# Optimization experiments

Measured on AMD Instinct MI355X. Metric: run time of the kernel, lower is better.

The kernel has to match this reference:

```python
import jax, jax.numpy as jnp
import numpy as np

G = 16          # grid_size
B = 2           # num graphs
SPACING = 1.5   # anchor_spacing
KA = 8          # atom_k_neighbors
KG = 24         # k_neighbors (grid->atom)
CUTOFF = 8.0
T = 16          # n_atom_types
H = 240         # hidden irreps dim (64x0e+32x1o+16x2e)
A = 9           # SH attr dim, lmax=2
C = 32          # code_dim
L = 2           # num_layers
BIG = 1e9

# real spherical harmonics, 'integral' normalization, e3nn component order
C0 = 0.28209479177387814   # 1/(2 sqrt(pi))
C1 = 0.4886025119029199    # sqrt(3/(4 pi))
C2A = 1.0925484305920792   # sqrt(15/(4 pi))
C2B = 0.31539156525252005  # sqrt(5/(16 pi))
C2C = 0.5462742152960396   # sqrt(15/(16 pi))

def _sph(rel, dist):
    u = rel / jnp.maximum(dist, 1e-9)[:, None]
    x, y, z = u[:, 0], u[:, 1], u[:, 2]
    return jnp.stack([
        jnp.full_like(x, C0),
        C1 * y, C1 * z, C1 * x,
        C2A * x * y, C2A * y * z, C2B * (3.0 * z * z - 1.0),
        C2A * z * x, C2C * (x * x - y * y),
    ], axis=-1)


def setup_inputs():
    key = jax.random.key(0)
    ks = jax.random.split(key, 12)
    Na = 1024
    half = G * SPACING / 2.0
    pos = jax.random.uniform(ks[0], (Na, 3), minval=-half, maxval=half, dtype=jnp.float32)
    atom_types = jax.random.randint(ks[1], (Na,), 0, T, dtype=jnp.int32)
    atom_batch = jnp.repeat(jnp.arange(B, dtype=jnp.int32), Na // B)

    def lin(k, shape):
        fan_in = shape[-2]
        return jax.random.normal(k, shape, dtype=jnp.float32) / jnp.sqrt(float(fan_in))

    Din = 2 * H + A
    return dict(
        pos=pos, atom_types=atom_types, atom_batch=atom_batch,
        We=lin(ks[2], (T + A, H)), be=jnp.zeros((H,), jnp.float32),
        Wm1=lin(ks[3], (L, Din, H)), bm1=jnp.zeros((L, H), jnp.float32),
        Wm2=lin(ks[4], (L, H, H)), bm2=jnp.zeros((L, H), jnp.float32),
        Wu1=lin(ks[5], (L, Din, H)), bu1=jnp.zeros((L, H), jnp.float32),
        Wu2=lin(ks[6], (L, H, H)), bu2=jnp.zeros((L, H), jnp.float32),
        Wo1=lin(ks[7], (H, H)), bo1=jnp.zeros((H,), jnp.float32),
        Wo2=lin(ks[8], (H, C)), bo2=jnp.zeros((C,), jnp.float32),
    )


def _forward(pos, atom_types, atom_batch, We, be, Wm1, bm1, Wm2, bm2,
             Wu1, bu1, Wu2, bu2, Wo1, bo1, Wo2, bo2):
    Na = pos.shape[0]
    ng = G ** 3
    Ng = B * ng
    N = Na + Ng

    # anchor grid, centered, spacing SPACING
    ax = (jnp.arange(G, dtype=pos.dtype) - (G - 1) / 2.0) * SPACING
    grid = jnp.stack(jnp.meshgrid(ax, ax, ax, indexing='ij'), -1).reshape(-1, 3)  # [ng,3]
    grid_flat = jnp.tile(grid, (B, 1))                                            # [Ng,3]
    grid_batch = jnp.repeat(jnp.arange(B, dtype=atom_batch.dtype), ng)
    node_pos = jnp.concatenate([pos, grid_flat], 0)                               # [N,3]

    # atom-atom knn_graph (no self loops, per-graph)
    d2 = jnp.sum((pos[:, None] - pos[None]) ** 2, -1)                             # [Na,Na]
    d2 = jnp.where(atom_batch[:, None] == atom_batch[None], d2, BIG)
    d2 = jnp.where(jnp.eye(Na, dtype=bool), BIG, d2)
    _, nbr = jax.lax.top_k(-d2, KA)                                               # [Na,KA]

    # grid->atom knn (per-graph), edge src=atom, dst=grid node
    d2g = jnp.sum((grid_flat[:, None] - pos[None]) ** 2, -1)                      # [Ng,Na]
    d2g = jnp.where(grid_batch[:, None] == atom_batch[None], d2g, BIG)
    _, nbg = jax.lax.top_k(-d2g, KG)                                              # [Ng,KG]

    src = jnp.concatenate([nbr.reshape(-1), nbg.reshape(-1)])
    dst = jnp.concatenate([jnp.repeat(jnp.arange(Na), KA),
                           Na + jnp.repeat(jnp.arange(Ng), KG)])

    rel = node_pos[src] - node_pos[dst]
    dist = jnp.linalg.norm(rel, axis=-1)
    mask = (dist <= CUTOFF).astype(pos.dtype)        # cutoff as mask (jit-friendly)
    ea = _sph(rel, dist) * mask[:, None]             # [E,A]

    # node attrs: scatter-mean of edge SH over destination nodes
    na_sum = jax.ops.segment_sum(ea, dst, num_segments=N)
    cnt = jax.ops.segment_sum(mask, dst, num_segments=N)
    node_attr = na_sum / jnp.maximum(cnt, 1.0)[:, None]
    node_attr = node_attr.at[:, 0].set(1.0)

    # node features: one-hot atoms, zeros for anchors
    feat = jnp.concatenate([jax.nn.one_hot(atom_types, T, dtype=pos.dtype),
                            jnp.zeros((Ng, T), pos.dtype)], 0)
    h = jax.nn.silu(jnp.concatenate([feat, node_attr], -1) @ We + be)

    # SEGNN-style message passing (attr-conditioned MLPs, masked-sum aggregation)
    for l in range(L):
        mi = jnp.concatenate([h[src], h[dst], ea], -1)                            # [E,2H+A]
        m = jax.nn.silu(jax.nn.silu(mi @ Wm1[l] + bm1[l]) @ Wm2[l] + bm2[l])
        m = m * mask[:, None]
        agg = jax.ops.segment_sum(m, dst, num_segments=N)                         # [N,H]
        ui = jnp.concatenate([h, agg, node_attr], -1)                             # [N,2H+A]
        h = h + jax.nn.silu(jax.nn.silu(ui @ Wu1[l] + bu1[l]) @ Wu2[l] + bu2[l])

    out = jax.nn.silu(h @ Wo1 + bo1) @ Wo2 + bo2                                  # [N,C]
    return out[Na:].reshape(B, ng, C)


def reference(pos, atom_types, atom_batch, We, be, Wm1, bm1, Wm2, bm2,
              Wu1, bu1, Wu2, bu2, Wo1, bo1, Wo2, bo2):
    return _forward(pos, atom_types, atom_batch, We, be, Wm1, bm1, Wm2, bm2,
                    Wu1, bu1, Wu2, bu2, Wo1, bo1, Wo2, bo2)
```

## Files before the change

### kernel.cpp

```cpp
#include <hip/hip_runtime.h>
#include <math.h>

#define NA   1024
#define NGRID 4096
#define NB   2
#define NG   (NB*NGRID)
#define NN   (NA+NG)
#define KAK  8
#define KGK  24
#define EAE  (NA*KAK)
#define EGE  (NG*KGK)
#define ET   (EAE+EGE)
#define HD   240
#define TT   16
#define DIN  489
#define CD   32
#define CUTF 8.0f

typedef __attribute__((ext_vector_type(8))) short short8;
typedef __attribute__((ext_vector_type(4))) short short4v;
typedef __attribute__((ext_vector_type(4))) float f32x4;
typedef __attribute__((ext_vector_type(4))) int i32x4;

__device__ __forceinline__ float silu_f(float x) {
    return x / (1.0f + __expf(-x));
}
__device__ __forceinline__ short f2bf(float x) {
    unsigned u = __float_as_uint(x);
    unsigned r = (u + 0x7FFFu + ((u >> 16) & 1u)) >> 16;
    return (short)r;
}
__device__ __forceinline__ float bf2f(short s) {
    return __uint_as_float(((unsigned)(unsigned short)s) << 16);
}
__device__ __forceinline__ unsigned cvt_pk_bf16(float lo, float hi) {
    unsigned r;
    asm("v_cvt_pk_bf16_f32 %0, %1, %2" : "=v"(r) : "v"(lo), "v"(hi));
    return r;
}

template <int K>
__device__ __forceinline__ void wave_topk(unsigned long long key[8], int lane,
                                          int* __restrict__ outp) {
    unsigned long long lmin = key[0];
#pragma unroll
    for (int s = 1; s < 8; ++s) lmin = key[s] < lmin ? key[s] : lmin;
    int myout = -1;
    for (int t = 0; t < K; ++t) {
        unsigned long long m = lmin;
#pragma unroll
        for (int d = 1; d < 64; d <<= 1) {
            unsigned long long o = __shfl_xor(m, d);
            m = o < m ? o : m;
        }
        if (lane == t) myout = (int)(m & 1023u);
        if (m == lmin) {
#pragma unroll
            for (int s = 0; s < 8; ++s) if (key[s] == m) key[s] = ~0ull;
            lmin = key[0];
#pragma unroll
            for (int s = 1; s < 8; ++s) lmin = key[s] < lmin ? key[s] : lmin;
        }
    }
    if (lane < K) outp[lane] = myout;
}

__global__ __launch_bounds__(256) void knn_atoms_kernel(const float* __restrict__ pos,
                                                        int* __restrict__ nbr) {
    __shared__ float sx[512], sy[512], sz[512];
    int tid = threadIdx.x;
    int q0 = blockIdx.x * 4;
    int pbase = (q0 >= 512) ? 512 : 0;
    for (int j = tid; j < 512; j += 256) {
        sx[j] = pos[(pbase + j)*3 + 0];
        sy[j] = pos[(pbase + j)*3 + 1];
        sz[j] = pos[(pbase + j)*3 + 2];
    }
    __syncthreads();
    int lane = tid & 63;
    int i = q0 + (tid >> 6);
    float px = sx[i - pbase], py = sy[i - pbase], pz = sz[i - pbase];
    unsigned long long key[8];
#pragma unroll
    for (int s = 0; s < 8; ++s) {
        int c = s * 64 + lane;
        int j = pbase + c;
        float dx = px - sx[c], dy = py - sy[c], dz = pz - sz[c];
        float d2 = __fadd_rn(__fadd_rn(__fmul_rn(dx,dx), __fmul_rn(dy,dy)), __fmul_rn(dz,dz));
        key[s] = ((unsigned long long)__float_as_uint(d2) << 10) | (unsigned)j;
        if (j == i) key[s] = ~0ull;
    }
    wave_topk<KAK>(key, lane, &nbr[i*KAK]);
}

__global__ __launch_bounds__(256) void knn_grid_kernel(const float* __restrict__ pos,
                                                       int* __restrict__ nbg) {
    __shared__ float sx[512], sy[512], sz[512];
    int tid = threadIdx.x;
    int q0 = blockIdx.x * 4;
    int pbase = (q0 >= NGRID) ? 512 : 0;
    for (int j = tid; j < 512; j += 256) {
        sx[j] = pos[(pbase + j)*3 + 0];
        sy[j] = pos[(pbase + j)*3 + 1];
        sz[j] = pos[(pbase + j)*3 + 2];
    }
    __syncthreads();
    int lane = tid & 63;
    int g = q0 + (tid >> 6);
    int gi = g & (NGRID - 1);
    int ix = gi >> 8, iy = (gi >> 4) & 15, iz = gi & 15;
    float px = ((float)ix - 7.5f) * 1.5f;
    float py = ((float)iy - 7.5f) * 1.5f;
    float pz = ((float)iz - 7.5f) * 1.5f;
    unsigned long long key[8];
#pragma unroll
    for (int s = 0; s < 8; ++s) {
        int c = s * 64 + lane;
        int j = pbase + c;
        float dx = px - sx[c], dy = py - sy[c], dz = pz - sz[c];
        float d2 = __fadd_rn(__fadd_rn(__fmul_rn(dx,dx), __fmul_rn(dy,dy)), __fmul_rn(dz,dz));
        key[s] = ((unsigned long long)__float_as_uint(d2) << 10) | (unsigned)j;
    }
    wave_topk<KGK>(key, lane, &nbg[g*KGK]);
}

__global__ void edge_kernel(const float* __restrict__ pos, const int* __restrict__ nbr,
                            const int* __restrict__ nbg, float* __restrict__ ea,
                            float* __restrict__ emask) {
    int e = blockIdx.x * blockDim.x + threadIdx.x;
    if (e >= ET) return;
    int src; float dpx, dpy, dpz;
    if (e < EAE) {
        int d = e >> 3;
        src = nbr[e];
        dpx = pos[d*3]; dpy = pos[d*3+1]; dpz = pos[d*3+2];
    } else {
        int eg = e - EAE;
        src = nbg[eg];
        int gg = eg / KGK;
        int gi = gg % NGRID;
        int ix = gi >> 8, iy = (gi >> 4) & 15, iz = gi & 15;
        dpx = ((float)ix - 7.5f) * 1.5f;
        dpy = ((float)iy - 7.5f) * 1.5f;
        dpz = ((float)iz - 7.5f) * 1.5f;
    }
    float rx = pos[src*3] - dpx, ry = pos[src*3+1] - dpy, rz = pos[src*3+2] - dpz;
    float dist = sqrtf(rx*rx + ry*ry + rz*rz);
    float mask = (dist <= CUTF) ? 1.0f : 0.0f;
    float inv = 1.0f / fmaxf(dist, 1e-9f);
    float x = rx * inv, y = ry * inv, z = rz * inv;
    float s0 = 0.28209479177387814f;
    float s1 = 0.4886025119029199f * y;
    float s2 = 0.4886025119029199f * z;
    float s3 = 0.4886025119029199f * x;
    float s4 = 1.0925484305920792f * x * y;
    float s5 = 1.0925484305920792f * y * z;
    float s6 = 0.31539156525252005f * (3.0f * z * z - 1.0f);
    float s7 = 1.0925484305920792f * z * x;
    float s8 = 0.5462742152960396f * (x * x - y * y);
    float* o = &ea[(size_t)e * 12];
    float4 o0 = {s0*mask, s1*mask, s2*mask, s3*mask};
    float4 o1 = {s4*mask, s5*mask, s6*mask, s7*mask};
    float4 o2 = {s8*mask, 0.f, 0.f, 0.f};
    *(float4*)(o)     = o0;
    *(float4*)(o + 4) = o1;
    *(float4*)(o + 8) = o2;
    emask[e] = mask;
}

__global__ void node_attr_kernel(const float* __restrict__ ea, const float* __restrict__ emask,
                                 float* __restrict__ attr) {
    int n = blockIdx.x * blockDim.x + threadIdx.x;
    if (n >= NN) return;
    int K, e0;
    if (n < NA) { K = KAK; e0 = n * KAK; }
    else        { K = KGK; e0 = EAE + (n - NA) * KGK; }
    float s[9];
#pragma unroll
    for (int a = 0; a < 9; ++a) s[a] = 0.f;
    float cnt = 0.f;
    for (int k = 0; k < K; ++k) {
        cnt += emask[e0 + k];
        const float* p = &ea[(size_t)(e0 + k) * 12];
#pragma unroll
        for (int a = 0; a < 9; ++a) s[a] += p[a];
    }
    float invc = 1.0f / fmaxf(cnt, 1.0f);
    attr[n*9+0] = 1.0f;
#pragma unroll
    for (int a = 1; a < 9; ++a) attr[n*9+a] = s[a] * invc;
}

__global__ void encoder_kernel(const int* __restrict__ types, const float* __restrict__ attr,
                               const float* __restrict__ We, const float* __restrict__ be,
                               float* __restrict__ h) {
    int idx = blockIdx.x * blockDim.x + threadIdx.x;
    int n = idx / HD, j = idx % HD;
    float acc = be[j];
    if (n < NA) acc += We[types[n] * HD + j];
#pragma unroll
    for (int a = 0; a < 9; ++a) acc += attr[n*9+a] * We[(TT + a) * HD + j];
    h[idx] = silu_f(acc);
}

__global__ void convert_w_kernel(const float* __restrict__ src, short* __restrict__ dst,
                                 int K, int Kpad) {
    int idx = blockIdx.x * blockDim.x + threadIdx.x;
    int per = 256 * Kpad;
    int l = idx / per;
    int rem = idx % per;
    int col = rem / Kpad, k = rem % Kpad;
    short v = 0;
    if (k < K && col < 240) v = f2bf(src[(size_t)l * K * 240 + (size_t)k * 240 + col]);
    dst[idx] = v;
}

__global__ void convert_wm1hl_kernel(const float* __restrict__ Wm1, short* __restrict__ hi,
                                     short* __restrict__ lo, int rowoff) {
    int idx = blockIdx.x * blockDim.x + threadIdx.x;
    int l = idx >> 16;
    int rem = idx & 65535;
    int col = rem >> 8, k = rem & 255;
    float v = 0.f;
    if (k < 240 && col < 240) v = Wm1[(size_t)l * DIN * HD + (size_t)(rowoff + k) * HD + col];
    short h16 = f2bf(v);
    hi[idx] = h16;
    lo[idx] = f2bf(v - bf2f(h16));
}

__global__ __launch_bounds__(256) void node_z_mfma_kernel(
        const float* __restrict__ h,
        const short* __restrict__ wzd_hi, const short* __restrict__ wzd_lo,
        const short* __restrict__ wzs_hi, const short* __restrict__ wzs_lo,
        const float* __restrict__ bm1,
        float* __restrict__ Zs, float* __restrict__ Zd) {
    __shared__ __align__(16) short Ahi[32 * 256];
    __shared__ __align__(16) short Alo[32 * 256];
    int tid = threadIdx.x;
    int n0 = blockIdx.x * 32;

#pragma unroll
    for (int it = 0; it < 4; ++it) {
        int idx = it * 256 + tid;
        int row = idx >> 5, q = idx & 31;
        int j = q * 8;
        short8 ohi = {0,0,0,0,0,0,0,0}, olo = {0,0,0,0,0,0,0,0};
        if (j < 240) {
            const float4 a0 = *(const float4*)(h + (size_t)(n0 + row) * HD + j);
            const float4 a1 = *(const float4*)(h + (size_t)(n0 + row) * HD + j + 4);
            float v[8] = {a0.x, a0.y, a0.z, a0.w, a1.x, a1.y, a1.z, a1.w};
#pragma unroll
            for (int a = 0; a < 8; ++a) {
                short hh = f2bf(v[a]);
                ohi[a] = hh;
                olo[a] = f2bf(v[a] - bf2f(hh));
            }
        }
        int boff = row * 512 + ((q * 16) ^ ((row & 7) << 4));
        *(short8*)((char*)Ahi + boff) = ohi;
        *(short8*)((char*)Alo + boff) = olo;
    }
    __syncthreads();

    int wid = tid >> 6, lane = tid & 63;
    int mw = wid >> 1, nw = wid & 1;
    int lg = lane >> 4, lc = lane & 15;
    int col0 = nw * 128;
    int arow = (mw * 16 + lc) * 256;

    f32x4 acc[8];
#pragma unroll
    for (int nt = 0; nt < 8; ++nt) acc[nt] = (f32x4){0.f, 0.f, 0.f, 0.f};
#pragma unroll
    for (int kc = 0; kc < 8; ++kc) {
        int aoff = arow + ((kc * 32 + lg * 8) ^ ((lc & 7) << 3));
        const short8 ahi = *(const short8*)&Ahi[aoff];
        const short8 alo = *(const short8*)&Alo[aoff];
#pragma unroll
        for (int nt = 0; nt < 8; ++nt) {
            size_t bo = (size_t)(col0 + nt*16 + lc) * 256 + kc*32 + lg*8;
            const short8 bhi = *(const short8*)(wzd_hi + bo);
            const short8 blo = *(const short8*)(wzd_lo + bo);
            acc[nt] = __builtin_amdgcn_mfma_f32_16x16x32_bf16(ahi, bhi, acc[nt], 0, 0, 0);
            acc[nt] = __builtin_amdgcn_mfma_f32_16x16x32_bf16(ahi, blo, acc[nt], 0, 0, 0);
            acc[nt] = __builtin_amdgcn_mfma_f32_16x16x32_bf16(alo, bhi, acc[nt], 0, 0, 0);
        }
    }
#pragma unroll
    for (int nt = 0; nt < 8; ++nt) {
        int ncol = col0 + nt * 16 + lc;
        if (ncol < HD) {
            float bias = bm1[ncol];
            float vals[4] = {acc[nt].x, acc[nt].y, acc[nt].z, acc[nt].w};
#pragma unroll
            for (int r = 0; r < 4; ++r)
                Zd[(size_t)(n0 + mw*16 + lg*4 + r) * HD + ncol] = vals[r] + bias;
        }
    }

    if (n0 < NA) {
#pragma unroll
        for (int nt = 0; nt < 8; ++nt) acc[nt] = (f32x4){0.f, 0.f, 0.f, 0.f};
#pragma unroll
        for (int kc = 0; kc < 8; ++kc) {
            int aoff = arow + ((kc * 32 + lg * 8) ^ ((lc & 7) << 3));
            const short8 ahi = *(const short8*)&Ahi[aoff];
            const short8 alo = *(const short8*)&Alo[aoff];
#pragma unroll
            for (int nt = 0; nt < 8; ++nt) {
                size_t bo = (size_t)(col0 + nt*16 + lc) * 256 + kc*32 + lg*8;
                const short8 bhi = *(const short8*)(wzs_hi + bo);
                const short8 blo = *(const short8*)(wzs_lo + bo);
                acc[nt] = __builtin_amdgcn_mfma_f32_16x16x32_bf16(ahi, bhi, acc[nt], 0, 0, 0);
                acc[nt] = __builtin_amdgcn_mfma_f32_16x16x32_bf16(ahi, blo, acc[nt], 0, 0, 0);
                acc[nt] = __builtin_amdgcn_mfma_f32_16x16x32_bf16(alo, bhi, acc[nt], 0, 0, 0);
            }
        }
#pragma unroll
        for (int nt = 0; nt < 8; ++nt) {
            int ncol = col0 + nt * 16 + lc;
            if (ncol < HD) {
                float vals[4] = {acc[nt].x, acc[nt].y, acc[nt].z, acc[nt].w};
#pragma unroll
                for (int r = 0; r < 4; ++r)
                    Zs[(size_t)(n0 + mw*16 + lg*4 + r) * HD + ncol] = vals[r];
            }
        }
    }
}

__global__ __launch_bounds__(256) void msg_gemm_kernel(
        const float* __restrict__ Zs, const float* __restrict__ Zd,
        const int* __restrict__ nbg, const float* __restrict__ ea,
        const float* __restrict__ emask, const float* __restrict__ Wea,
        const short* __restrict__ wm2t, const float* __restrict__ bm2,
        float* __restrict__ agg) {
    __shared__ __align__(16) short Abuf[48 * 256];
    __shared__ __align__(16) float mkbuf[48];
    int tid = threadIdx.x;
    int blk = blockIdx.x;
    int e0 = blk * 48;

    int q = tid & 31;
    int rh = tid >> 5;
    float4 w0[9], w1[9];
    int srcs[6];
    if (q < 30) {
        int j = q * 8;
#pragma unroll
        for (int a = 0; a < 9; ++a) {
            w0[a] = *(const float4*)(Wea + a * HD + j);
            w1[a] = *(const float4*)(Wea + a * HD + j + 4);
        }
#pragma unroll
        for (int r8 = 0; r8 < 6; ++r8) srcs[r8] = nbg[e0 + rh + r8 * 8];
    }
    if (tid < 48) mkbuf[tid] = emask[EAE + e0 + tid];

#pragma unroll
    for (int r8 = 0; r8 < 6; ++r8) {
        int row = rh + r8 * 8;
        i32x4 oi = (i32x4){0, 0, 0, 0};
        if (q < 30) {
            int j = q * 8;
            int eg = e0 + row;
            int srcn = srcs[r8];
            int dstn = NA + blk * 2 + ((r8 >= 3) ? 1 : 0);
            const float4 zs0 = *(const float4*)(Zs + (size_t)srcn * HD + j);
            const float4 zs1 = *(const float4*)(Zs + (size_t)srcn * HD + j + 4);
            const float4 zd0 = *(const float4*)(Zd + (size_t)dstn * HD + j);
            const float4 zd1 = *(const float4*)(Zd + (size_t)dstn * HD + j + 4);
            float s0 = zs0.x + zd0.x, s1 = zs0.y + zd0.y, s2 = zs0.z + zd0.z, s3 = zs0.w + zd0.w;
            float s4 = zs1.x + zd1.x, s5 = zs1.y + zd1.y, s6 = zs1.z + zd1.z, s7 = zs1.w + zd1.w;
            const float* ep = ea + (size_t)(EAE + eg) * 12;
            const float4 ev0 = *(const float4*)(ep);
            const float4 ev1 = *(const float4*)(ep + 4);
            const float  ev8 = ep[8];
            float ev[9] = {ev0.x, ev0.y, ev0.z, ev0.w, ev1.x, ev1.y, ev1.z, ev1.w, ev8};
#pragma unroll
            for (int a = 0; a < 9; ++a) {
                float e = ev[a];
                s0 += e * w0[a].x; s1 += e * w0[a].y; s2 += e * w0[a].z; s3 += e * w0[a].w;
                s4 += e * w1[a].x; s5 += e * w1[a].y; s6 += e * w1[a].z; s7 += e * w1[a].w;
            }
            oi[0] = (int)cvt_pk_bf16(silu_f(s0), silu_f(s1));
            oi[1] = (int)cvt_pk_bf16(silu_f(s2), silu_f(s3));
            oi[2] = (int)cvt_pk_bf16(silu_f(s4), silu_f(s5));
            oi[3] = (int)cvt_pk_bf16(silu_f(s6), silu_f(s7));
        }
        *(i32x4*)((char*)Abuf + row * 512 + ((q * 16) ^ ((row & 7) << 4))) = oi;
    }
    __syncthreads();

    int wid = tid >> 6, lane = tid & 63;
    int lg = lane >> 4, lc = lane & 15;
    int col0 = wid * 64;

    f32x4 acc[3][4];
#pragma unroll
    for (int mt = 0; mt < 3; ++mt)
#pragma unroll
        for (int nt = 0; nt < 4; ++nt) acc[mt][nt] = (f32x4){0.f, 0.f, 0.f, 0.f};

#pragma unroll
    for (int kc = 0; kc < 8; ++kc) {
        short8 af[3];
#pragma unroll
        for (int mt = 0; mt < 3; ++mt)
            af[mt] = *(const short8*)&Abuf[(mt*16 + lc) * 256 +
                                           ((kc*32 + lg*8) ^ ((lc & 7) << 3))];
#pragma unroll
        for (int nt = 0; nt < 4; ++nt) {
            const short8 bf = *(const short8*)(wm2t + (size_t)(col0 + nt*16 + lc) * 256 + kc*32 + lg*8);
#pragma unroll
            for (int mt = 0; mt < 3; ++mt)
                acc[mt][nt] = __builtin_amdgcn_mfma_f32_16x16x32_bf16(af[mt], bf, acc[mt][nt], 0, 0, 0);
        }
    }

#pragma unroll
    for (int nt = 0; nt < 4; ++nt) {
        int ncol = col0 + nt * 16 + lc;
        float bias = (ncol < HD) ? bm2[ncol] : 0.f;
        float p[3];
#pragma unroll
        for (int mt = 0; mt < 3; ++mt) {
            const float4 mkv = *(const float4*)&mkbuf[mt*16 + lg*4];
            float t0 = silu_f(acc[mt][nt].x + bias) * mkv.x;
            float t1 = silu_f(acc[mt][nt].y + bias) * mkv.y;
            float t2 = silu_f(acc[mt][nt].z + bias) * mkv.z;
            float t3 = silu_f(acc[mt][nt].w + bias) * mkv.w;
            p[mt] = (t0 + t1) + (t2 + t3);
        }
        float v0 = p[0] + ((lg < 2) ? p[1] : 0.f);
        float v1 = ((lg >= 2) ? p[1] : 0.f) + p[2];
        v0 += __shfl_xor(v0, 16); v0 += __shfl_xor(v0, 32);
        v1 += __shfl_xor(v1, 16); v1 += __shfl_xor(v1, 32);
        if (ncol < HD) {
            int node = NA + blk * 2;
            if (lane < 16)      agg[(size_t)(node + 0) * HD + ncol] = v0;
            else if (lane < 32) agg[(size_t)(node + 1) * HD + ncol] = v1;
        }
    }
}

template <int KE, int NPB>
__global__ __launch_bounds__(192) void msg_mfma_kernel(
        const float* __restrict__ Zs, const float* __restrict__ Zd,
        const int* __restrict__ nbrList, const float* __restrict__ ea,
        const float* __restrict__ emask, const float* __restrict__ Wea,
        const short* __restrict__ wm2t, const float* __restrict__ bm2,
        float* __restrict__ agg, int dstBase, int edgeBase) {
    constexpr int ROWS = KE * NPB;
    constexpr int MT = ROWS / 16;
    __shared__ __align__(16) short Abuf[ROWS * 264];
    __shared__ __align__(16) float mkbuf[ROWS];

    int tid = threadIdx.x;
    int b = blockIdx.x;
    int e0 = edgeBase + b * ROWS;

    if (tid < ROWS) mkbuf[tid] = emask[e0 + tid];
    for (int idx = tid; idx < ROWS * 24; idx += 192) {
        int r = idx / 24;
        Abuf[r * 264 + 240 + (idx % 24)] = 0;
    }
    for (int idx = tid; idx < ROWS * 60; idx += 192) {
        int row = idx / 60;
        int j = (idx % 60) * 4;
        int srcn = nbrList[b * ROWS + row];
        int dstn = dstBase + b * NPB + row / KE;
        const float4 zs = *(const float4*)(Zs + (size_t)srcn * HD + j);
        const float4 zd = *(const float4*)(Zd + (size_t)dstn * HD + j);
        float s0 = zs.x + zd.x, s1 = zs.y + zd.y, s2 = zs.z + zd.z, s3 = zs.w + zd.w;
        const float* ep = ea + (size_t)(e0 + row) * 12;
#pragma unroll
        for (int a = 0; a < 9; ++a) {
            float ev = ep[a];
            const float4 w = *(const float4*)(Wea + a * HD + j);
            s0 += ev * w.x; s1 += ev * w.y; s2 += ev * w.z; s3 += ev * w.w;
        }
        short4v o;
        o.x = f2bf(silu_f(s0)); o.y = f2bf(silu_f(s1));
        o.z = f2bf(silu_f(s2)); o.w = f2bf(silu_f(s3));
        *(short4v*)&Abuf[row * 264 + j] = o;
    }
    __syncthreads();

    int w = tid / 64, lane = tid % 64;
    int lg = lane >> 4, lc = lane & 15;
    int wcol0 = w * 80;

    f32x4 acc[MT][5];
#pragma unroll
    for (int mt = 0; mt < MT; ++mt)
#pragma unroll
        for (int nt = 0; nt < 5; ++nt) acc[mt][nt] = (f32x4){0.f, 0.f, 0.f, 0.f};

#pragma unroll
    for (int kc = 0; kc < 8; ++kc) {
        short8 af[MT];
#pragma unroll
        for (int mt = 0; mt < MT; ++mt)
            af[mt] = *(const short8*)&Abuf[(mt * 16 + lc) * 264 + kc * 32 + lg * 8];
#pragma unroll
        for (int nt = 0; nt < 5; ++nt) {
            const short8 bf = *(const short8*)(wm2t + (size_t)(wcol0 + nt * 16 + lc) * 256 + kc * 32 + lg * 8);
#pragma unroll
            for (int mt = 0; mt < MT; ++mt)
                acc[mt][nt] = __builtin_amdgcn_mfma_f32_16x16x32_bf16(af[mt], bf, acc[mt][nt], 0, 0, 0);
        }
    }

#pragma unroll
    for (int nt = 0; nt < 5; ++nt) {
        int ncol = wcol0 + nt * 16 + lc;
        float bias = bm2[ncol];
        float p[MT];
#pragma unroll
        for (int mt = 0; mt < MT; ++mt) {
            const float4 mkv = *(const float4*)&mkbuf[mt * 16 + lg * 4];
            float t0 = silu_f(acc[mt][nt].x + bias) * mkv.x;
            float t1 = silu_f(acc[mt][nt].y + bias) * mkv.y;
            float t2 = silu_f(acc[mt][nt].z + bias) * mkv.z;
            float t3 = silu_f(acc[mt][nt].w + bias) * mkv.w;
            p[mt] = (t0 + t1) + (t2 + t3);
        }
#pragma unroll
        for (int mt = 0; mt < MT; ++mt) {
            float v = p[mt];
            v += __shfl_xor(v, 16);
            if (lane < 16)
                agg[(size_t)(dstBase + b * (2 * MT) + 2 * mt + 0) * HD + ncol] = v;
            else if (lane >= 32 && lane < 48)
                agg[(size_t)(dstBase + b * (2 * MT) + 2 * mt + 1) * HD + ncol] = v;
        }
    }
}

__global__ __launch_bounds__(256) void update_mfma_kernel(
        float* __restrict__ h, const float* __restrict__ agg,
        const float* __restrict__ attr,
        const short* __restrict__ wu1t, const float* __restrict__ bu1,
        const short* __restrict__ wu2t, const float* __restrict__ bu2) {
    __shared__ __align__(16) short Abuf[32 * 512];
    __shared__ __align__(16) short Ubuf[32 * 256];
    int tid = threadIdx.x;
    int n0 = blockIdx.x * 32;

#pragma unroll
    for (int it = 0; it < 8; ++it) {
        int idx = it * 256 + tid;
        int row = idx >> 6, q = idx & 63;
        int j = q * 8;
        int n = n0 + row;
        short8 o = {0,0,0,0,0,0,0,0};
        if (j < 240) {
            const float4 a0 = *(const float4*)(h + (size_t)n * HD + j);
            const float4 a1 = *(const float4*)(h + (size_t)n * HD + j + 4);
            o[0]=f2bf(a0.x); o[1]=f2bf(a0.y); o[2]=f2bf(a0.z); o[3]=f2bf(a0.w);
            o[4]=f2bf(a1.x); o[5]=f2bf(a1.y); o[6]=f2bf(a1.z); o[7]=f2bf(a1.w);
        } else if (j < 480) {
            const float4 a0 = *(const float4*)(agg + (size_t)n * HD + (j - 240));
            const float4 a1 = *(const float4*)(agg + (size_t)n * HD + (j - 240) + 4);
            o[0]=f2bf(a0.x); o[1]=f2bf(a0.y); o[2]=f2bf(a0.z); o[3]=f2bf(a0.w);
            o[4]=f2bf(a1.x); o[5]=f2bf(a1.y); o[6]=f2bf(a1.z); o[7]=f2bf(a1.w);
        } else if (j == 480) {
#pragma unroll
            for (int a = 0; a < 8; ++a) o[a] = f2bf(attr[n*9 + a]);
        } else if (j == 488) {
            o[0] = f2bf(attr[n*9 + 8]);
        }
        *(short8*)((char*)Abuf + row * 1024 + ((q * 16) ^ ((row & 7) << 4))) = o;
    }
    __syncthreads();

    int wid = tid >> 6, lane = tid & 63;
    int mw = wid >> 1, nw = wid & 1;
    int lg = lane >> 4, lc = lane & 15;
    int col0 = nw * 128;

    f32x4 acc[8];
#pragma unroll
    for (int nt = 0; nt < 8; ++nt) acc[nt] = (f32x4){0.f, 0.f, 0.f, 0.f};
#pragma unroll
    for (int kc = 0; kc < 16; ++kc) {
        const short8 af = *(const short8*)((char*)Abuf + (mw*16 + lc) * 1024 +
                                           ((kc*64 + lg*16) ^ ((lc & 7) << 4)));
#pragma unroll
        for (int nt = 0; nt < 8; ++nt) {
            const short8 bf = *(const short8*)(wu1t + (size_t)(col0 + nt*16 + lc) * 512 + kc*32 + lg*8);
            acc[nt] = __builtin_amdgcn_mfma_f32_16x16x32_bf16(af, bf, acc[nt], 0, 0, 0);
        }
    }
#pragma unroll
    for (int nt = 0; nt < 8; ++nt) {
        int ncol = col0 + nt * 16 + lc;
        float bias = (ncol < HD) ? bu1[ncol] : 0.f;
        float vals[4] = {acc[nt].x, acc[nt].y, acc[nt].z, acc[nt].w};
#pragma unroll
        for (int r = 0; r < 4; ++r) {
            int row = mw*16 + lg*4 + r;
            *(short*)((char*)Ubuf + row * 512 + ((ncol * 2) ^ ((row & 7) << 4))) =
                f2bf(silu_f(vals[r] + bias));
        }
    }
    __syncthreads();

    f32x4 acc2[8];
#pragma unroll
    for (int nt = 0; nt < 8; ++nt) acc2[nt] = (f32x4){0.f, 0.f, 0.f, 0.f};
#pragma unroll
    for (int kc = 0; kc < 8; ++kc) {
        const short8 af = *(const short8*)((char*)Ubuf + (mw*16 + lc) * 512 +
                                           ((kc*64 + lg*16) ^ ((lc & 7) << 4)));
#pragma unroll
        for (int nt = 0; nt < 8; ++nt) {
            const short8 bf = *(const short8*)(wu2t + (size_t)(col0 + nt*16 + lc) * 256 + kc*32 + lg*8);
            acc2[nt] = __builtin_amdgcn_mfma_f32_16x16x32_bf16(af, bf, acc2[nt], 0, 0, 0);
        }
    }
#pragma unroll
    for (int nt = 0; nt < 8; ++nt) {
        int ncol = col0 + nt * 16 + lc;
        if (ncol < HD) {
            float bias = bu2[ncol];
            float vals[4] = {acc2[nt].x, acc2[nt].y, acc2[nt].z, acc2[nt].w};
#pragma unroll
            for (int r = 0; r < 4; ++r) {
                int row = mw*16 + lg*4 + r;
                size_t hi = (size_t)(n0 + row) * HD + ncol;
                h[hi] += silu_f(vals[r] + bias);
            }
        }
    }
}

__global__ void output_kernel(const float* __restrict__ h,
                              const float* __restrict__ Wo1, const float* __restrict__ bo1,
                              const float* __restrict__ Wo2, const float* __restrict__ bo2,
                              float* __restrict__ out) {
    const int NBT = 4;
    __shared__ float hr[NBT][HD];
    __shared__ float o1[NBT][HD];
    int tid = threadIdx.x;
    int g0 = blockIdx.x * NBT;
    for (int idx = tid; idx < NBT * HD; idx += 256) {
        int k = idx / HD, i = idx % HD;
        hr[k][i] = h[(size_t)(NA + g0 + k) * HD + i];
    }
    __syncthreads();
    int j = tid;
    if (j < HD) {
        float acc[NBT] = {0.f, 0.f, 0.f, 0.f};
        for (int i4 = 0; i4 < 60; ++i4) {
            int i = 4 * i4;
            float w0 = Wo1[(i+0)*HD+j], w1 = Wo1[(i+1)*HD+j];
            float w2 = Wo1[(i+2)*HD+j], w3 = Wo1[(i+3)*HD+j];
#pragma unroll
            for (int k = 0; k < NBT; ++k) {
                const float4 a = *reinterpret_cast<const float4*>(&hr[k][i]);
                acc[k] += a.x*w0 + a.y*w1 + a.z*w2 + a.w*w3;
            }
        }
        float bb = bo1[j];
#pragma unroll
        for (int k = 0; k < NBT; ++k) o1[k][j] = silu_f(acc[k] + bb);
    }
    __syncthreads();
    if (tid < NBT * CD) {
        int k = tid >> 5, c = tid & 31;
        float acc = bo2[c];
        for (int i = 0; i < HD; ++i) acc += o1[k][i] * Wo2[i*CD + c];
        out[(size_t)(g0 + k) * CD + c] = acc;
    }
}

extern "C" void kernel_launch(void* const* d_in, const int* in_sizes, int n_in,
                              void* d_out, int out_size, void* d_ws, size_t ws_size,
                              hipStream_t stream) {
    (void)in_sizes; (void)n_in; (void)out_size; (void)ws_size;
    const float* pos   = (const float*)d_in[0];
    const int*   types = (const int*)d_in[1];
    const int*   batch = (const int*)d_in[2];
    (void)batch;
    const float* We    = (const float*)d_in[3];
    const float* be    = (const float*)d_in[4];
    const float* Wm1   = (const float*)d_in[5];
    const float* bm1   = (const float*)d_in[6];
    const float* Wm2   = (const float*)d_in[7];
    const float* bm2   = (const float*)d_in[8];
    const float* Wu1   = (const float*)d_in[9];
    const float* bu1   = (const float*)d_in[10];
    const float* Wu2   = (const float*)d_in[11];
    const float* bu2   = (const float*)d_in[12];
    const float* Wo1   = (const float*)d_in[13];
    const float* bo1   = (const float*)d_in[14];
    const float* Wo2   = (const float*)d_in[15];
    const float* bo2   = (const float*)d_in[16];
    float* out = (float*)d_out;

    char* ws = (char*)d_ws;
    size_t off = 0;
    auto take = [&](size_t bytes) -> char* {
        char* p = ws + off;
        off = (off + bytes + 255) & ~(size_t)255;
        return p;
    };
    int*   nbr    = (int*)take((size_t)EAE * 4);
    int*   nbg    = (int*)take((size_t)EGE * 4);
    float* ea     = (float*)take((size_t)ET * 12 * 4);
    float* emask  = (float*)take((size_t)ET * 4);
    float* attr   = (float*)take((size_t)NN * 9 * 4);
    float* h      = (float*)take((size_t)NN * HD * 4);
    float* agg    = (float*)take((size_t)NN * HD * 4);
    float* zs     = (float*)take((size_t)NA * HD * 4);
    float* zd     = (float*)take((size_t)NN * HD * 4);
    short* wm2t   = (short*)take((size_t)2 * 256 * 256 * 2);
    short* wu1t   = (short*)take((size_t)2 * 256 * 512 * 2);
    short* wu2t   = (short*)take((size_t)2 * 256 * 256 * 2);
    short* wzd_hi = (short*)take((size_t)2 * 256 * 256 * 2);
    short* wzd_lo = (short*)take((size_t)2 * 256 * 256 * 2);
    short* wzs_hi = (short*)take((size_t)2 * 256 * 256 * 2);
    short* wzs_lo = (short*)take((size_t)2 * 256 * 256 * 2);

    knn_atoms_kernel<<<NA/4, 256, 0, stream>>>(pos, nbr);
    knn_grid_kernel<<<NG/4, 256, 0, stream>>>(pos, nbg);
    edge_kernel<<<ET/256, 256, 0, stream>>>(pos, nbr, nbg, ea, emask);
    node_attr_kernel<<<NN/256, 256, 0, stream>>>(ea, emask, attr);
    encoder_kernel<<<(NN*HD)/256, 256, 0, stream>>>(types, attr, We, be, h);
    convert_w_kernel<<<(2*256*256)/256, 256, 0, stream>>>(Wm2, wm2t, 240, 256);
    convert_w_kernel<<<(2*256*512)/256, 256, 0, stream>>>(Wu1, wu1t, DIN, 512);
    convert_w_kernel<<<(2*256*256)/256, 256, 0, stream>>>(Wu2, wu2t, 240, 256);
    convert_wm1hl_kernel<<<(2*256*256)/256, 256, 0, stream>>>(Wm1, wzd_hi, wzd_lo, 240);
    convert_wm1hl_kernel<<<(2*256*256)/256, 256, 0, stream>>>(Wm1, wzs_hi, wzs_lo, 0);

    for (int l = 0; l < 2; ++l) {
        const float* wm1 = Wm1 + (size_t)l * DIN * HD;
        const float* wea = wm1 + (size_t)480 * HD;
        const short* w2t = wm2t + (size_t)l * 256 * 256;
        const float* bb2 = bm2 + l * HD;
        node_z_mfma_kernel<<<NN/32, 256, 0, stream>>>(
            h,
            wzd_hi + (size_t)l * 65536, wzd_lo + (size_t)l * 65536,
            wzs_hi + (size_t)l * 65536, wzs_lo + (size_t)l * 65536,
            bm1 + l * HD, zs, zd);
        msg_mfma_kernel<KAK, 8><<<NA*KAK/64, 192, 0, stream>>>(
            zs, zd, nbr, ea, emask, wea, w2t, bb2, agg, 0, 0);
        msg_gemm_kernel<<<EGE/48, 256, 0, stream>>>(zs, zd, nbg, ea, emask, wea, w2t, bb2, agg);
        update_mfma_kernel<<<NN/32, 256, 0, stream>>>(
            h, agg, attr,
            wu1t + (size_t)l * 256 * 512, bu1 + l * HD,
            wu2t + (size_t)l * 256 * 256, bu2 + l * HD);
    }
    output_kernel<<<NG/4, 256, 0, stream>>>(h, Wo1, bo1, Wo2, bo2, out);
}
```

Before: 661.5 us.

## Merge kNN and weight-conversion launches, pack edge attrs to 9 floats, hoist Zd loads

Combines the atom and grid kNN kernels into one launch and the five weight-conversion kernels into a single kernel, cutting launch count and per-launch overhead. Edge attributes are stored with a stride of 9 floats instead of 12, which shrinks that buffer but replaces the aligned float4 accesses with scalar ones. In the grid message kernel, the two destination Zd rows are loaded once per thread up front rather than reloaded for every row.

Result: faster. 626.0 us (-5.4%).

```diff
diff --git a/kernel.cpp b/kernel.cpp
--- a/kernel.cpp
+++ b/kernel.cpp
@@ -65,12 +65,16 @@
     if (lane < K) outp[lane] = myout;
 }
 
-__global__ __launch_bounds__(256) void knn_atoms_kernel(const float* __restrict__ pos,
-                                                        int* __restrict__ nbr) {
+__global__ __launch_bounds__(256) void knn_kernel(const float* __restrict__ pos,
+                                                  int* __restrict__ nbr,
+                                                  int* __restrict__ nbg) {
     __shared__ float sx[512], sy[512], sz[512];
     int tid = threadIdx.x;
-    int q0 = blockIdx.x * 4;
-    int pbase = (q0 >= 512) ? 512 : 0;
+    bool isAtom = blockIdx.x < (NA / 4);
+    int q0 = isAtom ? blockIdx.x * 4 : (blockIdx.x - NA / 4) * 4;
+    int pbase;
+    if (isAtom) pbase = (q0 >= 512) ? 512 : 0;
+    else        pbase = (q0 >= NGRID) ? 512 : 0;
     for (int j = tid; j < 512; j += 256) {
         sx[j] = pos[(pbase + j)*3 + 0];
         sy[j] = pos[(pbase + j)*3 + 1];
@@ -78,50 +82,39 @@
     }
     __syncthreads();
     int lane = tid & 63;
-    int i = q0 + (tid >> 6);
-    float px = sx[i - pbase], py = sy[i - pbase], pz = sz[i - pbase];
-    unsigned long long key[8];
-#pragma unroll
-    for (int s = 0; s < 8; ++s) {
-        int c = s * 64 + lane;
-        int j = pbase + c;
-        float dx = px - sx[c], dy = py - sy[c], dz = pz - sz[c];
-        float d2 = __fadd_rn(__fadd_rn(__fmul_rn(dx,dx), __fmul_rn(dy,dy)), __fmul_rn(dz,dz));
-        key[s] = ((unsigned long long)__float_as_uint(d2) << 10) | (unsigned)j;
-        if (j == i) key[s] = ~0ull;
-    }
-    wave_topk<KAK>(key, lane, &nbr[i*KAK]);
-}
-
-__global__ __launch_bounds__(256) void knn_grid_kernel(const float* __restrict__ pos,
-                                                       int* __restrict__ nbg) {
-    __shared__ float sx[512], sy[512], sz[512];
-    int tid = threadIdx.x;
-    int q0 = blockIdx.x * 4;
-    int pbase = (q0 >= NGRID) ? 512 : 0;
-    for (int j = tid; j < 512; j += 256) {
-        sx[j] = pos[(pbase + j)*3 + 0];
-        sy[j] = pos[(pbase + j)*3 + 1];
-        sz[j] = pos[(pbase + j)*3 + 2];
-    }
-    __syncthreads();
-    int lane = tid & 63;
-    int g = q0 + (tid >> 6);
-    int gi = g & (NGRID - 1);
-    int ix = gi >> 8, iy = (gi >> 4) & 15, iz = gi & 15;
-    float px = ((float)ix - 7.5f) * 1.5f;
-    float py = ((float)iy - 7.5f) * 1.5f;
-    float pz = ((float)iz - 7.5f) * 1.5f;
-    unsigned long long key[8];
-#pragma unroll
-    for (int s = 0; s < 8; ++s) {
-        int c = s * 64 + lane;
-        int j = pbase + c;
-        float dx = px - sx[c], dy = py - sy[c], dz = pz - sz[c];
-        float d2 = __fadd_rn(__fadd_rn(__fmul_rn(dx,dx), __fmul_rn(dy,dy)), __fmul_rn(dz,dz));
-        key[s] = ((unsigned long long)__float_as_uint(d2) << 10) | (unsigned)j;
-    }
-    wave_topk<KGK>(key, lane, &nbg[g*KGK]);
+    int qq = q0 + (tid >> 6);
+    if (isAtom) {
+        int i = qq;
+        float px = sx[i - pbase], py = sy[i - pbase], pz = sz[i - pbase];
+        unsigned long long key[8];
+#pragma unroll
+        for (int s = 0; s < 8; ++s) {
+            int c = s * 64 + lane;
+            int j = pbase + c;
+            float dx = px - sx[c], dy = py - sy[c], dz = pz - sz[c];
+            float d2 = __fadd_rn(__fadd_rn(__fmul_rn(dx,dx), __fmul_rn(dy,dy)), __fmul_rn(dz,dz));
+            key[s] = ((unsigned long long)__float_as_uint(d2) << 10) | (unsigned)j;
+            if (j == i) key[s] = ~0ull;
+        }
+        wave_topk<KAK>(key, lane, &nbr[i*KAK]);
+    } else {
+        int g = qq;
+        int gi = g & (NGRID - 1);
+        int ix = gi >> 8, iy = (gi >> 4) & 15, iz = gi & 15;
+        float px = ((float)ix - 7.5f) * 1.5f;
+        float py = ((float)iy - 7.5f) * 1.5f;
+        float pz = ((float)iz - 7.5f) * 1.5f;
+        unsigned long long key[8];
+#pragma unroll
+        for (int s = 0; s < 8; ++s) {
+            int c = s * 64 + lane;
+            int j = pbase + c;
+            float dx = px - sx[c], dy = py - sy[c], dz = pz - sz[c];
+            float d2 = __fadd_rn(__fadd_rn(__fmul_rn(dx,dx), __fmul_rn(dy,dy)), __fmul_rn(dz,dz));
+            key[s] = ((unsigned long long)__float_as_uint(d2) << 10) | (unsigned)j;
+        }
+        wave_topk<KGK>(key, lane, &nbg[g*KGK]);
+    }
 }
 
 __global__ void edge_kernel(const float* __restrict__ pos, const int* __restrict__ nbr,
@@ -158,13 +151,9 @@
     float s6 = 0.31539156525252005f * (3.0f * z * z - 1.0f);
     float s7 = 1.0925484305920792f * z * x;
     float s8 = 0.5462742152960396f * (x * x - y * y);
-    float* o = &ea[(size_t)e * 12];
-    float4 o0 = {s0*mask, s1*mask, s2*mask, s3*mask};
-    float4 o1 = {s4*mask, s5*mask, s6*mask, s7*mask};
-    float4 o2 = {s8*mask, 0.f, 0.f, 0.f};
-    *(float4*)(o)     = o0;
-    *(float4*)(o + 4) = o1;
-    *(float4*)(o + 8) = o2;
+    float* o = &ea[(size_t)e * 9];
+    o[0] = s0 * mask; o[1] = s1 * mask; o[2] = s2 * mask; o[3] = s3 * mask;
+    o[4] = s4 * mask; o[5] = s5 * mask; o[6] = s6 * mask; o[7] = s7 * mask; o[8] = s8 * mask;
     emask[e] = mask;
 }
 
@@ -181,7 +170,7 @@
     float cnt = 0.f;
     for (int k = 0; k < K; ++k) {
         cnt += emask[e0 + k];
-        const float* p = &ea[(size_t)(e0 + k) * 12];
+        const float* p = &ea[(size_t)(e0 + k) * 9];
 #pragma unroll
         for (int a = 0; a < 9; ++a) s[a] += p[a];
     }
@@ -203,29 +192,47 @@
     h[idx] = silu_f(acc);
 }
 
-__global__ void convert_w_kernel(const float* __restrict__ src, short* __restrict__ dst,
-                                 int K, int Kpad) {
+__global__ void convert_all_kernel(const float* __restrict__ Wm2, const float* __restrict__ Wu1,
+                                   const float* __restrict__ Wu2, const float* __restrict__ Wm1,
+                                   short* __restrict__ wm2t, short* __restrict__ wu1t,
+                                   short* __restrict__ wu2t,
+                                   short* __restrict__ wzd_hi, short* __restrict__ wzd_lo,
+                                   short* __restrict__ wzs_hi, short* __restrict__ wzs_lo) {
     int idx = blockIdx.x * blockDim.x + threadIdx.x;
-    int per = 256 * Kpad;
-    int l = idx / per;
-    int rem = idx % per;
-    int col = rem / Kpad, k = rem % Kpad;
-    short v = 0;
-    if (k < K && col < 240) v = f2bf(src[(size_t)l * K * 240 + (size_t)k * 240 + col]);
-    dst[idx] = v;
-}
-
-__global__ void convert_wm1hl_kernel(const float* __restrict__ Wm1, short* __restrict__ hi,
-                                     short* __restrict__ lo, int rowoff) {
-    int idx = blockIdx.x * blockDim.x + threadIdx.x;
-    int l = idx >> 16;
-    int rem = idx & 65535;
-    int col = rem >> 8, k = rem & 255;
-    float v = 0.f;
-    if (k < 240 && col < 240) v = Wm1[(size_t)l * DIN * HD + (size_t)(rowoff + k) * HD + col];
-    short h16 = f2bf(v);
-    hi[idx] = h16;
-    lo[idx] = f2bf(v - bf2f(h16));
+    if (idx < 131072) {
+        int l = idx >> 16, rem = idx & 65535, col = rem >> 8, k = rem & 255;
+        short v = 0;
+        if (k < 240 && col < 240) v = f2bf(Wm2[(size_t)l*57600 + k*240 + col]);
+        wm2t[idx] = v;
+    } else if (idx < 393216) {
+        int i = idx - 131072;
+        int l = i / 131072, rem = i % 131072, col = rem >> 9, k = rem & 511;
+        short v = 0;
+        if (k < DIN && col < 240) v = f2bf(Wu1[(size_t)l*DIN*240 + (size_t)k*240 + col]);
+        wu1t[i] = v;
+    } else if (idx < 524288) {
+        int i = idx - 393216;
+        int l = i >> 16, rem = i & 65535, col = rem >> 8, k = rem & 255;
+        short v = 0;
+        if (k < 240 && col < 240) v = f2bf(Wu2[(size_t)l*57600 + k*240 + col]);
+        wu2t[i] = v;
+    } else if (idx < 655360) {
+        int i = idx - 524288;
+        int l = i >> 16, rem = i & 65535, col = rem >> 8, k = rem & 255;
+        float v = 0.f;
+        if (k < 240 && col < 240) v = Wm1[(size_t)l*DIN*HD + (size_t)(240 + k)*HD + col];
+        short hh = f2bf(v);
+        wzd_hi[i] = hh;
+        wzd_lo[i] = f2bf(v - bf2f(hh));
+    } else {
+        int i = idx - 655360;
+        int l = i >> 16, rem = i & 65535, col = rem >> 8, k = rem & 255;
+        float v = 0.f;
+        if (k < 240 && col < 240) v = Wm1[(size_t)l*DIN*HD + (size_t)k*HD + col];
+        short hh = f2bf(v);
+        wzs_hi[i] = hh;
+        wzs_lo[i] = f2bf(v - bf2f(hh));
+    }
 }
 
 __global__ __launch_bounds__(256) void node_z_mfma_kernel(
@@ -344,6 +351,7 @@
     int q = tid & 31;
     int rh = tid >> 5;
     float4 w0[9], w1[9];
+    float4 zdA0, zdA1, zdB0, zdB1;
     int srcs[6];
     if (q < 30) {
         int j = q * 8;
@@ -354,6 +362,11 @@
         }
 #pragma unroll
         for (int r8 = 0; r8 < 6; ++r8) srcs[r8] = nbg[e0 + rh + r8 * 8];
+        int dn0 = NA + blk * 2;
+        zdA0 = *(const float4*)(Zd + (size_t)dn0 * HD + j);
+        zdA1 = *(const float4*)(Zd + (size_t)dn0 * HD + j + 4);
+        zdB0 = *(const float4*)(Zd + (size_t)(dn0 + 1) * HD + j);
+        zdB1 = *(const float4*)(Zd + (size_t)(dn0 + 1) * HD + j + 4);
     }
     if (tid < 48) mkbuf[tid] = emask[EAE + e0 + tid];
 
@@ -365,21 +378,16 @@
             int j = q * 8;
             int eg = e0 + row;
             int srcn = srcs[r8];
-            int dstn = NA + blk * 2 + ((r8 >= 3) ? 1 : 0);
             const float4 zs0 = *(const float4*)(Zs + (size_t)srcn * HD + j);
             const float4 zs1 = *(const float4*)(Zs + (size_t)srcn * HD + j + 4);
-            const float4 zd0 = *(const float4*)(Zd + (size_t)dstn * HD + j);
-            const float4 zd1 = *(const float4*)(Zd + (size_t)dstn * HD + j + 4);
+            const float4 zd0 = (r8 < 3) ? zdA0 : zdB0;
+            const float4 zd1 = (r8 < 3) ? zdA1 : zdB1;
             float s0 = zs0.x + zd0.x, s1 = zs0.y + zd0.y, s2 = zs0.z + zd0.z, s3 = zs0.w + zd0.w;
             float s4 = zs1.x + zd1.x, s5 = zs1.y + zd1.y, s6 = zs1.z + zd1.z, s7 = zs1.w + zd1.w;
-            const float* ep = ea + (size_t)(EAE + eg) * 12;
-            const float4 ev0 = *(const float4*)(ep);
-            const float4 ev1 = *(const float4*)(ep + 4);
-            const float  ev8 = ep[8];
-            float ev[9] = {ev0.x, ev0.y, ev0.z, ev0.w, ev1.x, ev1.y, ev1.z, ev1.w, ev8};
+            const float* ep = ea + (size_t)(EAE + eg) * 9;
 #pragma unroll
             for (int a = 0; a < 9; ++a) {
-                float e = ev[a];
+                float e = ep[a];
                 s0 += e * w0[a].x; s1 += e * w0[a].y; s2 += e * w0[a].z; s3 += e * w0[a].w;
                 s4 += e * w1[a].x; s5 += e * w1[a].y; s6 += e * w1[a].z; s7 += e * w1[a].w;
             }
@@ -473,7 +481,7 @@
         const float4 zs = *(const float4*)(Zs + (size_t)srcn * HD + j);
         const float4 zd = *(const float4*)(Zd + (size_t)dstn * HD + j);
         float s0 = zs.x + zd.x, s1 = zs.y + zd.y, s2 = zs.z + zd.z, s3 = zs.w + zd.w;
-        const float* ep = ea + (size_t)(e0 + row) * 12;
+        const float* ep = ea + (size_t)(e0 + row) * 9;
 #pragma unroll
         for (int a = 0; a < 9; ++a) {
             float ev = ep[a];
@@ -709,7 +717,7 @@
     };
     int*   nbr    = (int*)take((size_t)EAE * 4);
     int*   nbg    = (int*)take((size_t)EGE * 4);
-    float* ea     = (float*)take((size_t)ET * 12 * 4);
+    float* ea     = (float*)take((size_t)ET * 9 * 4);
     float* emask  = (float*)take((size_t)ET * 4);
     float* attr   = (float*)take((size_t)NN * 9 * 4);
     float* h      = (float*)take((size_t)NN * HD * 4);
@@ -724,16 +732,13 @@
     short* wzs_hi = (short*)take((size_t)2 * 256 * 256 * 2);
     short* wzs_lo = (short*)take((size_t)2 * 256 * 256 * 2);
 
-    knn_atoms_kernel<<<NA/4, 256, 0, stream>>>(pos, nbr);
-    knn_grid_kernel<<<NG/4, 256, 0, stream>>>(pos, nbg);
+    knn_kernel<<<NA/4 + NG/4, 256, 0, stream>>>(pos, nbr, nbg);
     edge_kernel<<<ET/256, 256, 0, stream>>>(pos, nbr, nbg, ea, emask);
     node_attr_kernel<<<NN/256, 256, 0, stream>>>(ea, emask, attr);
     encoder_kernel<<<(NN*HD)/256, 256, 0, stream>>>(types, attr, We, be, h);
-    convert_w_kernel<<<(2*256*256)/256, 256, 0, stream>>>(Wm2, wm2t, 240, 256);
-    convert_w_kernel<<<(2*256*512)/256, 256, 0, stream>>>(Wu1, wu1t, DIN, 512);
-    convert_w_kernel<<<(2*256*256)/256, 256, 0, stream>>>(Wu2, wu2t, 240, 256);
-    convert_wm1hl_kernel<<<(2*256*256)/256, 256, 0, stream>>>(Wm1, wzd_hi, wzd_lo, 240);
-    convert_wm1hl_kernel<<<(2*256*256)/256, 256, 0, stream>>>(Wm1, wzs_hi, wzs_lo, 0);
+    convert_all_kernel<<<786432/256, 256, 0, stream>>>(Wm2, Wu1, Wu2, Wm1,
+                                                       wm2t, wu1t, wu2t,
+                                                       wzd_hi, wzd_lo, wzs_hi, wzs_lo);
 
     for (int l = 0; l < 2; ++l) {
         const float* wm1 = Wm1 + (size_t)l * DIN * HD;
```
